# Optimization experiments

Measured on AMD Instinct MI355X. Metric: run time of the kernel, lower is better.

## Reference

```python
import jax, jax.numpy as jnp
import numpy as np

H = 4  # num_heads

def setup_inputs() -> dict:
    key = jax.random.key(0)
    ks = jax.random.split(key, 9)
    B, S, D = 8, 2048, 256
    x = jax.random.normal(ks[0], (B, S, D), dtype=jnp.float32)
    scale = 1.0 / np.sqrt(D)
    Wq = jax.random.normal(ks[1], (D, D), dtype=jnp.float32) * scale
    bq = jnp.zeros((D,), dtype=jnp.float32)
    Wk = jax.random.normal(ks[2], (D, D), dtype=jnp.float32) * scale
    bk = jnp.zeros((D,), dtype=jnp.float32)
    Wv = jax.random.normal(ks[3], (D, D), dtype=jnp.float32) * scale
    bv = jnp.zeros((D,), dtype=jnp.float32)
    Wo = jax.random.normal(ks[4], (D, D), dtype=jnp.float32) * scale
    bo = jnp.zeros((D,), dtype=jnp.float32)
    return {"x": x, "Wq": Wq, "bq": bq, "Wk": Wk, "bk": bk,
            "Wv": Wv, "bv": bv, "Wo": Wo, "bo": bo}

def reference(x, Wq, bq, Wk, bk, Wv, bv, Wo, bo):
    B, S, D = x.shape
    hd = D // H
    inv_scale = 1.0 / jnp.sqrt(jnp.asarray(hd, x.dtype))
    # projections: torch Linear is x @ W.T + b; weights here stored as (D, D) used as x @ W + b
    def split_heads(t):
        return t.reshape(B, S, H, hd).transpose(0, 2, 1, 3)  # [B,H,S,hd]
    Q = split_heads(x @ Wq + bq)
    K = split_heads(x @ Wk + bk)
    V = split_heads(x @ Wv + bv)
    scores = jnp.einsum('bhqd,bhkd->bhqk', Q, K) * inv_scale  # [B,H,S,S]
    attn = jax.nn.softmax(scores, axis=-1)
    # dropout is identity in eval mode
    ctx = jnp.einsum('bhqk,bhkd->bhqd', attn, V)
    ctx = ctx.transpose(0, 2, 1, 3).reshape(B, S, D)
    return ctx @ Wo + bo
```

## Files before the change

### kernel.cpp

```cpp
#include <hip/hip_runtime.h>


typedef unsigned short u16;
typedef __bf16 bf16x8 __attribute__((ext_vector_type(8)));
typedef float  f32x4  __attribute__((ext_vector_type(4)));
typedef unsigned int u32x4 __attribute__((ext_vector_type(4)));
typedef unsigned int u32x2 __attribute__((ext_vector_type(2)));

#define LOG2E   1.4426950408889634f
#define ATTN_SC (0.125f * LOG2E)
#define PSTR    2097152
#define WPSTR   32768
#define WZSTR   65536

__device__ __forceinline__ u16 f2b(float f) {
  unsigned u = __builtin_bit_cast(unsigned, f);
  u += 0x7FFFu + ((u >> 16) & 1u);
  return (u16)(u >> 16);
}
__device__ __forceinline__ float b2f(u16 b) {
  return __builtin_bit_cast(float, (unsigned)b << 16);
}
__device__ __forceinline__ unsigned pack_trunc(float a, float b) {
  return (__builtin_bit_cast(unsigned, a) >> 16) | (__builtin_bit_cast(unsigned, b) & 0xFFFF0000u);
}
__device__ __forceinline__ unsigned pack_rne(float a, float b) {
  return (unsigned)f2b(a) | ((unsigned)f2b(b) << 16);
}
__device__ __forceinline__ f32x4 mfma16(bf16x8 a, bf16x8 b, f32x4 c) {
  return __builtin_amdgcn_mfma_f32_16x16x32_bf16(a, b, c, 0, 0, 0);
}
__device__ __forceinline__ void cp16(const u16* g, u16* l) {
  __builtin_amdgcn_global_load_lds((const __attribute__((address_space(1))) void*)g,
                                   (__attribute__((address_space(3))) void*)l, 16, 0, 0);
}

template <typename T>
__global__ __launch_bounds__(256) void prep(const T* __restrict__ x,
                                            const T* __restrict__ W0, const T* __restrict__ W1,
                                            const T* __restrict__ W2, const T* __restrict__ W3,
                                            const T* __restrict__ b0, const T* __restrict__ b1,
                                            const T* __restrict__ b2, const T* __restrict__ b3,
                                            u16* __restrict__ xp, u16* __restrict__ WTp,
                                            float* __restrict__ biasf) {
  int bid = blockIdx.x;
  if (bid < 4096) {
    int i0 = (bid * 256 + threadIdx.x) * 4;
    int row = i0 >> 8, col = i0 & 255;
    int p = col >> 7, pc = col & 127;
    u16* o = xp + (size_t)p * PSTR + (size_t)row * 128 + pc;
#pragma unroll
    for (int j = 0; j < 4; ++j) {
      if constexpr (sizeof(T) == 4) o[j] = f2b((float)x[i0 + j]);
      else                          o[j] = (u16)x[i0 + j];
    }
  } else {
    bid -= 4096;
    const int z = bid >> 8;
    const T* W = z == 0 ? W0 : z == 1 ? W1 : z == 2 ? W2 : W3;
    const T* b = z == 0 ? b0 : z == 1 ? b1 : z == 2 ? b2 : b3;
    int idx = (bid & 255) * 256 + threadIdx.x;
    int k = idx >> 8, n = idx & 255;
    u16 wb;
    if constexpr (sizeof(T) == 4) wb = f2b((float)W[k * 256 + n]);
    else                          wb = (u16)W[k * 256 + n];
    WTp[z * WZSTR + (k >> 7) * WPSTR + n * 128 + (k & 127)] = wb;
    if (idx < 256) {
      float bv;
      if constexpr (sizeof(T) == 4) bv = (float)b[idx];
      else                          bv = b2f((u16)b[idx]);
      biasf[z * 256 + idx] = bv;
    }
  }
}

__device__ __forceinline__ void gemm_body(const u16* Ab, const u16* Bb,
                                          u16* Al, u16* Bl, f32x4 acc[2][4], int tid) {
  const int w = tid >> 6, lane = tid & 63;
  const int l16 = lane & 15, quad = lane >> 4;
#pragma unroll
  for (int p = 0; p < 2; ++p) {
    __syncthreads();
    const u16* Ap = Ab + (size_t)p * PSTR;
    const u16* Bp = Bb + p * WPSTR;
#pragma unroll
    for (int i = 0; i < 8; ++i) {
      int slot = i * 256 + w * 64 + lane;
      int row = slot >> 4, pc = slot & 15, c = pc ^ (row & 15);
      cp16(Ap + (size_t)row * 128 + c * 8, Al + (i * 256 + w * 64) * 8);
    }
#pragma unroll
    for (int i = 0; i < 4; ++i) {
      int slot = i * 256 + w * 64 + lane;
      int row = slot >> 4, pc = slot & 15, c = pc ^ (row & 15);
      cp16(Bp + (size_t)row * 128 + c * 8, Bl + (i * 256 + w * 64) * 8);
    }
    __syncthreads();
#pragma unroll
    for (int kc = 0; kc < 4; ++kc) {
      bf16x8 a0 = *(const bf16x8*)&Al[(w * 32 + l16) * 128 + (((kc * 4 + quad) ^ l16)) * 8];
      bf16x8 a1 = *(const bf16x8*)&Al[(w * 32 + 16 + l16) * 128 + (((kc * 4 + quad) ^ l16)) * 8];
#pragma unroll
      for (int nb = 0; nb < 4; ++nb) {
        bf16x8 b = *(const bf16x8*)&Bl[(nb * 16 + l16) * 128 + (((kc * 4 + quad) ^ l16)) * 8];
        acc[0][nb] = mfma16(a0, b, acc[0][nb]);
        acc[1][nb] = mfma16(a1, b, acc[1][nb]);
      }
    }
  }
}

__global__ __launch_bounds__(256) void qkv_gemm(const u16* __restrict__ xp, const u16* __restrict__ WTp,
                                                const float* __restrict__ biasf,
                                                u16* __restrict__ Qw, u16* __restrict__ Kw,
                                                u16* __restrict__ VTg) {
  __shared__ __align__(16) u16 Al[128 * 128];
  __shared__ __align__(16) u16 Bl[64 * 128];
  const int tid = threadIdx.x, w = tid >> 6, lane = tid & 63;
  const int l16 = lane & 15, quad = lane >> 4;
  const int z = blockIdx.z, n0 = blockIdx.y * 64, m0 = blockIdx.x * 128;
  f32x4 acc[2][4];
#pragma unroll
  for (int mm = 0; mm < 2; ++mm)
#pragma unroll
    for (int nb = 0; nb < 4; ++nb) acc[mm][nb] = (f32x4){0.f, 0.f, 0.f, 0.f};

  gemm_body(xp + (size_t)m0 * 128, WTp + z * WZSTR + n0 * 128, Al, Bl, acc, tid);

  const float* bp = biasf + z * 256;
  const int bb = m0 >> 11, s0 = m0 & 2047, h = blockIdx.y;
  if (z < 2) {
    u16* dst = (z == 0) ? Qw : Kw;
    const float sc = (z == 0) ? ATTN_SC : 1.0f;
#pragma unroll
    for (int mm = 0; mm < 2; ++mm)
#pragma unroll
      for (int nb = 0; nb < 4; ++nb) {
        int d = nb * 16 + l16;
        float bv = bp[n0 + d];
#pragma unroll
        for (int r = 0; r < 4; ++r) {
          int s = s0 + w * 32 + mm * 16 + quad * 4 + r;
          dst[(((size_t)(bb * 4 + h) * 2048) + s) * 64 + d] = f2b((acc[mm][nb][r] + bv) * sc);
        }
      }
  } else {
    __syncthreads();
#pragma unroll
    for (int mm = 0; mm < 2; ++mm)
#pragma unroll
      for (int nb = 0; nb < 4; ++nb) {
        int d = nb * 16 + l16;
        float bv = bp[n0 + d];
        f32x4 v = acc[mm][nb];
        u32x2 dd = { pack_rne(v[0] + bv, v[1] + bv), pack_rne(v[2] + bv, v[3] + bv) };
        int cch = w * 4 + mm * 2 + (quad >> 1);
        *(u32x2*)&Bl[d * 128 + ((cch ^ (d & 15))) * 8 + (quad & 1) * 4] = dd;
      }
    __syncthreads();
#pragma unroll
    for (int i = 0; i < 4; ++i) {
      int slot = i * 256 + tid;
      int d = slot >> 4, pc = slot & 15;
      u32x4 vv = *(const u32x4*)&Bl[d * 128 + ((pc ^ (d & 15))) * 8];
      *(u32x4*)(VTg + (((size_t)(bb * 4 + h) * 64) + d) * 2048 + s0 + pc * 8) = vv;
    }
  }
}

template <bool OUT_BF16>
__global__ __launch_bounds__(256) void out_gemm(const u16* __restrict__ ctxp, const u16* __restrict__ WTp,
                                                const float* __restrict__ bo, void* __restrict__ outv) {
  __shared__ __align__(16) u16 Al[128 * 128];
  __shared__ __align__(16) u16 Bl[64 * 128];
  const int tid = threadIdx.x, w = tid >> 6, lane = tid & 63;
  const int l16 = lane & 15, quad = lane >> 4;
  const int n0 = blockIdx.y * 64, m0 = blockIdx.x * 128;
  f32x4 acc[2][4];
#pragma unroll
  for (int mm = 0; mm < 2; ++mm)
#pragma unroll
    for (int nb = 0; nb < 4; ++nb) acc[mm][nb] = (f32x4){0.f, 0.f, 0.f, 0.f};

  gemm_body(ctxp + (size_t)m0 * 128, WTp + 3 * WZSTR + n0 * 128, Al, Bl, acc, tid);

#pragma unroll
  for (int mm = 0; mm < 2; ++mm)
#pragma unroll
    for (int nb = 0; nb < 4; ++nb) {
      int n = n0 + nb * 16 + l16;
      float bv = bo[n];
#pragma unroll
      for (int r = 0; r < 4; ++r) {
        size_t m = m0 + w * 32 + mm * 16 + quad * 4 + r;
        float v = acc[mm][nb][r] + bv;
        if constexpr (OUT_BF16) ((u16*)outv)[m * 256 + n] = f2b(v);
        else                    ((float*)outv)[m * 256 + n] = v;
      }
    }
}

__global__ __launch_bounds__(256, 4) void attn(const u16* __restrict__ Q, const u16* __restrict__ K,
                                               const u16* __restrict__ VT, u16* __restrict__ ctxp) {
  __shared__ __align__(16) u16 Kt[2][64 * 64];
  __shared__ __align__(16) u16 VTt[2][64 * 64];
  __shared__ __align__(16) u16 Pt[4][16 * 64];
  const int tid = threadIdx.x;
  const int w = tid >> 6, lane = tid & 63;
  const int l16 = lane & 15, quad = lane >> 4;
  const int bh = blockIdx.y, q0 = blockIdx.x * 64;
  const u16* Qp = Q + (size_t)bh * 2048 * 64;
  const u16* Kp = K + (size_t)bh * 2048 * 64;
  const u16* Vp = VT + (size_t)bh * 64 * 2048;
  u16* Ptw = Pt[w];

  bf16x8 qf0, qf1;
  {
    int qrow = q0 + w * 16 + l16;
    qf0 = *(const bf16x8*)(Qp + (size_t)qrow * 64 + quad * 8);
    qf1 = *(const bf16x8*)(Qp + (size_t)qrow * 64 + 32 + quad * 8);
  }

  f32x4 acc[4];
#pragma unroll
  for (int nb = 0; nb < 4; ++nb) acc[nb] = (f32x4){0.f, 0.f, 0.f, 0.f};
  float dn = 0.f;

  const int sl0 = w * 64 + lane, sl1 = 256 + w * 64 + lane;
  const int r0 = sl0 >> 3, c0 = (sl0 & 7) ^ (r0 & 7);
  const int r1 = sl1 >> 3, c1 = (sl1 & 7) ^ (r1 & 7);

#define STAGE(kt_, buf_)                                                              \
  do {                                                                                \
    cp16(Kp + (size_t)((kt_) * 64 + r0) * 64 + c0 * 8, &Kt[buf_][(w * 64) * 8]);      \
    cp16(Kp + (size_t)((kt_) * 64 + r1) * 64 + c1 * 8, &Kt[buf_][(256 + w * 64) * 8]);\
    cp16(Vp + (size_t)r0 * 2048 + (kt_) * 64 + c0 * 8, &VTt[buf_][(w * 64) * 8]);     \
    cp16(Vp + (size_t)r1 * 2048 + (kt_) * 64 + c1 * 8, &VTt[buf_][(256 + w * 64) * 8]);\
  } while (0)

  STAGE(0, 0);

  for (int kt = 0; kt < 32; ++kt) {
    const int buf = kt & 1;
    __builtin_amdgcn_s_waitcnt(0x0F70 );
    __asm__ __volatile__("" ::: "memory");
    __builtin_amdgcn_s_barrier();
    __asm__ __volatile__("" ::: "memory");
    if (kt < 31) STAGE(kt + 1, buf ^ 1);

    const u16* KtB = Kt[buf];
    const u16* VtB = VTt[buf];

    bf16x8 vbr[2][4];
#pragma unroll
    for (int m = 0; m < 2; ++m)
#pragma unroll
      for (int nbD = 0; nbD < 4; ++nbD)
        vbr[m][nbD] = *(const bf16x8*)&VtB[(nbD * 16 + l16) * 64 + (((m * 4 + quad) ^ (l16 & 7))) * 8];

    f32x4 st[4];
#pragma unroll
    for (int nb = 0; nb < 4; ++nb) st[nb] = (f32x4){0.f, 0.f, 0.f, 0.f};
#pragma unroll
    for (int kc = 0; kc < 2; ++kc) {
      bf16x8 qb = kc ? qf1 : qf0;
#pragma unroll
      for (int nbK = 0; nbK < 4; ++nbK) {
        bf16x8 a = *(const bf16x8*)&KtB[(nbK * 16 + l16) * 64 + (((kc * 4 + quad) ^ (l16 & 7))) * 8];
        st[nbK] = mfma16(a, qb, st[nbK]);
      }
    }

#pragma unroll
    for (int nbK = 0; nbK < 4; ++nbK) {
      float p0 = exp2f(st[nbK][0]), p1 = exp2f(st[nbK][1]);
      float p2 = exp2f(st[nbK][2]), p3 = exp2f(st[nbK][3]);
      dn += (p0 + p1) + (p2 + p3);
      u32x2 dd = { pack_trunc(p0, p1), pack_trunc(p2, p3) };
      int cch = nbK * 2 + (quad >> 1);
      *(u32x2*)&Ptw[l16 * 64 + ((cch ^ (l16 & 7))) * 8 + (quad & 1) * 4] = dd;
    }

#pragma unroll
    for (int m = 0; m < 2; ++m) {
      bf16x8 pb = *(const bf16x8*)&Ptw[l16 * 64 + (((m * 4 + quad) ^ (l16 & 7))) * 8];
#pragma unroll
      for (int nbD = 0; nbD < 4; ++nbD)
        acc[nbD] = mfma16(vbr[m][nbD], pb, acc[nbD]);
    }
  }
#undef STAGE

  dn += __shfl_xor(dn, 16);
  dn += __shfl_xor(dn, 32);
  float linv = 1.0f / dn;

  __asm__ __volatile__("" ::: "memory");
  __builtin_amdgcn_s_barrier();
  __asm__ __volatile__("" ::: "memory");
#pragma unroll
  for (int nbD = 0; nbD < 4; ++nbD) {
    f32x4 v = acc[nbD];
    u32x2 dd = { pack_rne(v[0] * linv, v[1] * linv), pack_rne(v[2] * linv, v[3] * linv) };
    int cch = nbD * 2 + (quad >> 1);
    *(u32x2*)&Ptw[l16 * 64 + ((cch ^ (l16 & 7))) * 8 + (quad & 1) * 4] = dd;
  }
  const int bb = bh >> 2, h = bh & 3;
  const int p = h >> 1, pcol = (h & 1) * 64;
#pragma unroll
  for (int cc = 0; cc < 2; ++cc) {
    int slot = cc * 64 + lane;
    int row = slot >> 3, pc = slot & 7;
    u32x4 vv = *(const u32x4*)&Ptw[row * 64 + ((pc ^ (row & 7))) * 8];
    size_t m = (size_t)bb * 2048 + q0 + w * 16 + row;
    *(u32x4*)&ctxp[(size_t)p * PSTR + m * 128 + pcol + pc * 8] = vv;
  }
}

extern "C" void kernel_launch(void* const* d_in, const int* in_sizes, int n_in,
                              void* d_out, int out_size, void* d_ws, size_t ws_size,
                              hipStream_t stream) {
  bool f32in = true;
  {
    void* basep = nullptr; size_t sz = 0;
    hipError_t e = hipMemGetAddressRange((hipDeviceptr_t*)&basep, &sz, (hipDeviceptr_t)d_in[0]);
    if (e == hipSuccess && sz > 0) f32in = sz >= (size_t)in_sizes[0] * 4;
    else f32in = false;
  }

  char* ws = (char*)d_ws;
  u16*   xp    = (u16*)(ws + 0);
  u16*   ctxp  = xp;
  u16*   WTp   = (u16*)(ws + 8388608);
  float* biasf = (float*)(ws + 8912896);
  u16*   Qw    = (u16*)(ws + 8916992);
  u16*   Kw    = (u16*)(ws + 17305600);
  u16*   VTg   = (u16*)(ws + 25694208);

  dim3 blk(256);
  if (f32in) {
    prep<float><<<5120, blk, 0, stream>>>(
        (const float*)d_in[0],
        (const float*)d_in[1], (const float*)d_in[3], (const float*)d_in[5], (const float*)d_in[7],
        (const float*)d_in[2], (const float*)d_in[4], (const float*)d_in[6], (const float*)d_in[8],
        xp, WTp, biasf);
  } else {
    prep<u16><<<5120, blk, 0, stream>>>(
        (const u16*)d_in[0],
        (const u16*)d_in[1], (const u16*)d_in[3], (const u16*)d_in[5], (const u16*)d_in[7],
        (const u16*)d_in[2], (const u16*)d_in[4], (const u16*)d_in[6], (const u16*)d_in[8],
        xp, WTp, biasf);
  }
  qkv_gemm<<<dim3(128, 4, 3), blk, 0, stream>>>(xp, WTp, biasf, Qw, Kw, VTg);
  attn<<<dim3(32, 32), blk, 0, stream>>>(Qw, Kw, VTg, ctxp);
  if (f32in) out_gemm<false><<<dim3(128, 4), blk, 0, stream>>>(ctxp, WTp, biasf + 3 * 256, d_out);
  else       out_gemm<true ><<<dim3(128, 4), blk, 0, stream>>>(ctxp, WTp, biasf + 3 * 256, d_out);
}
```

Before: 168.9 us.

## Process 128 queries per attention block and keep P in registers

Each attention wave now handles two 16-row query tiles, so K and V fragments loaded from shared memory are reused across 32 queries and the grid halves. K rows are loaded in a permuted order so that the score MFMA output layout matches the B-operand layout of the PV MFMA. This lets the probability tile stay in registers instead of taking an LDS round trip. It also switches to the raw exp2 builtin and lowers launch bounds to 2 blocks per CU, trading occupancy and register pressure for the added reuse.

```diff
diff --git a/kernel.cpp b/kernel.cpp
--- a/kernel.cpp
+++ b/kernel.cpp
@@ -200,7 +200,7 @@
     }
 }
 
-__global__ __launch_bounds__(256, 4) void attn(const u16* __restrict__ Q, const u16* __restrict__ K,
+__global__ __launch_bounds__(256, 2) void attn(const u16* __restrict__ Q, const u16* __restrict__ K,
                                                const u16* __restrict__ VT, u16* __restrict__ ctxp) {
   __shared__ __align__(16) u16 Kt[2][64 * 64];
   __shared__ __align__(16) u16 VTt[2][64 * 64];
@@ -208,33 +208,38 @@
   const int tid = threadIdx.x;
   const int w = tid >> 6, lane = tid & 63;
   const int l16 = lane & 15, quad = lane >> 4;
-  const int bh = blockIdx.y, q0 = blockIdx.x * 64;
+  const int bh = blockIdx.y, q0 = blockIdx.x * 128;
   const u16* Qp = Q + (size_t)bh * 2048 * 64;
   const u16* Kp = K + (size_t)bh * 2048 * 64;
   const u16* Vp = VT + (size_t)bh * 64 * 2048;
   u16* Ptw = Pt[w];
 
-  bf16x8 qf0, qf1;
-  {
-    int qrow = q0 + w * 16 + l16;
-    qf0 = *(const bf16x8*)(Qp + (size_t)qrow * 64 + quad * 8);
-    qf1 = *(const bf16x8*)(Qp + (size_t)qrow * 64 + 32 + quad * 8);
-  }
-
-  f32x4 acc[4];
-#pragma unroll
-  for (int nb = 0; nb < 4; ++nb) acc[nb] = (f32x4){0.f, 0.f, 0.f, 0.f};
-  float dn = 0.f;
+  bf16x8 qf[2][2];
+#pragma unroll
+  for (int h = 0; h < 2; ++h) {
+    int qrow = q0 + w * 32 + h * 16 + l16;
+    qf[h][0] = *(const bf16x8*)(Qp + (size_t)qrow * 64 + quad * 8);
+    qf[h][1] = *(const bf16x8*)(Qp + (size_t)qrow * 64 + 32 + quad * 8);
+  }
+
+  f32x4 acc[2][4];
+#pragma unroll
+  for (int h = 0; h < 2; ++h)
+#pragma unroll
+    for (int nb = 0; nb < 4; ++nb) acc[h][nb] = (f32x4){0.f, 0.f, 0.f, 0.f};
+  float dn0 = 0.f, dn1 = 0.f;
 
   const int sl0 = w * 64 + lane, sl1 = 256 + w * 64 + lane;
   const int r0 = sl0 >> 3, c0 = (sl0 & 7) ^ (r0 & 7);
   const int r1 = sl1 >> 3, c1 = (sl1 & 7) ^ (r1 & 7);
-
-#define STAGE(kt_, buf_)                                                              \
-  do {                                                                                \
-    cp16(Kp + (size_t)((kt_) * 64 + r0) * 64 + c0 * 8, &Kt[buf_][(w * 64) * 8]);      \
-    cp16(Kp + (size_t)((kt_) * 64 + r1) * 64 + c1 * 8, &Kt[buf_][(256 + w * 64) * 8]);\
-    cp16(Vp + (size_t)r0 * 2048 + (kt_) * 64 + c0 * 8, &VTt[buf_][(w * 64) * 8]);     \
+  const int pr0 = (r0 & 0x20) | ((r0 & 0x0C) << 1) | ((r0 & 0x10) >> 2) | (r0 & 3);
+  const int pr1 = (r1 & 0x20) | ((r1 & 0x0C) << 1) | ((r1 & 0x10) >> 2) | (r1 & 3);
+
+#define STAGE(kt_, buf_)                                                               \
+  do {                                                                                 \
+    cp16(Kp + (size_t)((kt_) * 64 + pr0) * 64 + c0 * 8, &Kt[buf_][(w * 64) * 8]);      \
+    cp16(Kp + (size_t)((kt_) * 64 + pr1) * 64 + c1 * 8, &Kt[buf_][(256 + w * 64) * 8]);\
+    cp16(Vp + (size_t)r0 * 2048 + (kt_) * 64 + c0 * 8, &VTt[buf_][(w * 64) * 8]);      \
     cp16(Vp + (size_t)r1 * 2048 + (kt_) * 64 + c1 * 8, &VTt[buf_][(256 + w * 64) * 8]);\
   } while (0)
 
@@ -251,6 +256,12 @@
     const u16* KtB = Kt[buf];
     const u16* VtB = VTt[buf];
 
+    bf16x8 kfr[2][4];
+#pragma unroll
+    for (int kc = 0; kc < 2; ++kc)
+#pragma unroll
+      for (int nbK = 0; nbK < 4; ++nbK)
+        kfr[kc][nbK] = *(const bf16x8*)&KtB[(nbK * 16 + l16) * 64 + (((kc * 4 + quad) ^ (l16 & 7))) * 8];
     bf16x8 vbr[2][4];
 #pragma unroll
     for (int m = 0; m < 2; ++m)
@@ -258,62 +269,67 @@
       for (int nbD = 0; nbD < 4; ++nbD)
         vbr[m][nbD] = *(const bf16x8*)&VtB[(nbD * 16 + l16) * 64 + (((m * 4 + quad) ^ (l16 & 7))) * 8];
 
-    f32x4 st[4];
-#pragma unroll
-    for (int nb = 0; nb < 4; ++nb) st[nb] = (f32x4){0.f, 0.f, 0.f, 0.f};
-#pragma unroll
-    for (int kc = 0; kc < 2; ++kc) {
-      bf16x8 qb = kc ? qf1 : qf0;
+#pragma unroll
+    for (int h = 0; h < 2; ++h) {
+      f32x4 st[4];
+#pragma unroll
+      for (int nb = 0; nb < 4; ++nb) st[nb] = (f32x4){0.f, 0.f, 0.f, 0.f};
+#pragma unroll
+      for (int kc = 0; kc < 2; ++kc)
+#pragma unroll
+        for (int nbK = 0; nbK < 4; ++nbK)
+          st[nbK] = mfma16(kfr[kc][nbK], qf[h][kc], st[nbK]);
+
+      unsigned pw[8];
+      float d = 0.f;
 #pragma unroll
       for (int nbK = 0; nbK < 4; ++nbK) {
-        bf16x8 a = *(const bf16x8*)&KtB[(nbK * 16 + l16) * 64 + (((kc * 4 + quad) ^ (l16 & 7))) * 8];
-        st[nbK] = mfma16(a, qb, st[nbK]);
-      }
-    }
-
-#pragma unroll
-    for (int nbK = 0; nbK < 4; ++nbK) {
-      float p0 = exp2f(st[nbK][0]), p1 = exp2f(st[nbK][1]);
-      float p2 = exp2f(st[nbK][2]), p3 = exp2f(st[nbK][3]);
-      dn += (p0 + p1) + (p2 + p3);
-      u32x2 dd = { pack_trunc(p0, p1), pack_trunc(p2, p3) };
-      int cch = nbK * 2 + (quad >> 1);
+        float p0 = __builtin_amdgcn_exp2f(st[nbK][0]);
+        float p1 = __builtin_amdgcn_exp2f(st[nbK][1]);
+        float p2 = __builtin_amdgcn_exp2f(st[nbK][2]);
+        float p3 = __builtin_amdgcn_exp2f(st[nbK][3]);
+        d += (p0 + p1) + (p2 + p3);
+        pw[nbK * 2]     = pack_trunc(p0, p1);
+        pw[nbK * 2 + 1] = pack_trunc(p2, p3);
+      }
+      if (h == 0) dn0 += d; else dn1 += d;
+      bf16x8 pb0 = __builtin_bit_cast(bf16x8, (u32x4){pw[0], pw[1], pw[2], pw[3]});
+      bf16x8 pb1 = __builtin_bit_cast(bf16x8, (u32x4){pw[4], pw[5], pw[6], pw[7]});
+
+#pragma unroll
+      for (int nbD = 0; nbD < 4; ++nbD) acc[h][nbD] = mfma16(vbr[0][nbD], pb0, acc[h][nbD]);
+#pragma unroll
+      for (int nbD = 0; nbD < 4; ++nbD) acc[h][nbD] = mfma16(vbr[1][nbD], pb1, acc[h][nbD]);
+    }
+  }
+#undef STAGE
+
+  float linv0, linv1;
+  { float d = dn0; d += __shfl_xor(d, 16); d += __shfl_xor(d, 32); linv0 = 1.0f / d; }
+  { float d = dn1; d += __shfl_xor(d, 16); d += __shfl_xor(d, 32); linv1 = 1.0f / d; }
+
+  const int bb = bh >> 2, hh = bh & 3;
+  const int p = hh >> 1, pcol = (hh & 1) * 64;
+#pragma unroll
+  for (int h = 0; h < 2; ++h) {
+    const float linv = h ? linv1 : linv0;
+#pragma unroll
+    for (int nbD = 0; nbD < 4; ++nbD) {
+      f32x4 v = acc[h][nbD];
+      u32x2 dd = { pack_rne(v[0] * linv, v[1] * linv), pack_rne(v[2] * linv, v[3] * linv) };
+      int cch = nbD * 2 + (quad >> 1);
       *(u32x2*)&Ptw[l16 * 64 + ((cch ^ (l16 & 7))) * 8 + (quad & 1) * 4] = dd;
     }
-
-#pragma unroll
-    for (int m = 0; m < 2; ++m) {
-      bf16x8 pb = *(const bf16x8*)&Ptw[l16 * 64 + (((m * 4 + quad) ^ (l16 & 7))) * 8];
-#pragma unroll
-      for (int nbD = 0; nbD < 4; ++nbD)
-        acc[nbD] = mfma16(vbr[m][nbD], pb, acc[nbD]);
-    }
-  }
-#undef STAGE
-
-  dn += __shfl_xor(dn, 16);
-  dn += __shfl_xor(dn, 32);
-  float linv = 1.0f / dn;
-
-  __asm__ __volatile__("" ::: "memory");
-  __builtin_amdgcn_s_barrier();
-  __asm__ __volatile__("" ::: "memory");
-#pragma unroll
-  for (int nbD = 0; nbD < 4; ++nbD) {
-    f32x4 v = acc[nbD];
-    u32x2 dd = { pack_rne(v[0] * linv, v[1] * linv), pack_rne(v[2] * linv, v[3] * linv) };
-    int cch = nbD * 2 + (quad >> 1);
-    *(u32x2*)&Ptw[l16 * 64 + ((cch ^ (l16 & 7))) * 8 + (quad & 1) * 4] = dd;
-  }
-  const int bb = bh >> 2, h = bh & 3;
-  const int p = h >> 1, pcol = (h & 1) * 64;
-#pragma unroll
-  for (int cc = 0; cc < 2; ++cc) {
-    int slot = cc * 64 + lane;
-    int row = slot >> 3, pc = slot & 7;
-    u32x4 vv = *(const u32x4*)&Ptw[row * 64 + ((pc ^ (row & 7))) * 8];
-    size_t m = (size_t)bb * 2048 + q0 + w * 16 + row;
-    *(u32x4*)&ctxp[(size_t)p * PSTR + m * 128 + pcol + pc * 8] = vv;
+    __asm__ __volatile__("" ::: "memory");
+#pragma unroll
+    for (int cc = 0; cc < 2; ++cc) {
+      int slot = cc * 64 + lane;
+      int row = slot >> 3, pc = slot & 7;
+      u32x4 vv = *(const u32x4*)&Ptw[row * 64 + ((pc ^ (row & 7))) * 8];
+      size_t m = (size_t)bb * 2048 + q0 + w * 32 + h * 16 + row;
+      *(u32x4*)&ctxp[(size_t)p * PSTR + m * 128 + pcol + pc * 8] = vv;
+    }
+    __asm__ __volatile__("" ::: "memory");
   }
 }
 
@@ -352,7 +368,7 @@
         xp, WTp, biasf);
   }
   qkv_gemm<<<dim3(128, 4, 3), blk, 0, stream>>>(xp, WTp, biasf, Qw, Kw, VTg);
-  attn<<<dim3(32, 32), blk, 0, stream>>>(Qw, Kw, VTg, ctxp);
+  attn<<<dim3(16, 32), blk, 0, stream>>>(Qw, Kw, VTg, ctxp);
   if (f32in) out_gemm<false><<<dim3(128, 4), blk, 0, stream>>>(ctxp, WTp, biasf + 3 * 256, d_out);
   else       out_gemm<true ><<<dim3(128, 4), blk, 0, stream>>>(ctxp, WTp, biasf + 3 * 256, d_out);
 }
```

Result: faster. 150.6 us (-10.8%).
